# Optimization experiments

Measured on AMD Instinct MI355X. Metric: run time of the kernel, lower is better.

## Reference

```python
import jax, jax.numpy as jnp
import numpy as np

N_USERS = 100000
N_ITEMS = 50000
N_NODES = N_USERS + N_ITEMS
LATENT = 64
NNZ = 6000000
N_LAYERS = 3
BATCH = 2048


def setup_inputs() -> dict:
    key = jax.random.key(0)
    k1, k2, k3, k4, k5, k6, k7 = jax.random.split(key, 7)
    row_idx = jax.random.randint(k1, (NNZ,), 0, N_NODES, dtype=jnp.int64 if jax.config.jax_enable_x64 else jnp.int32)
    col_idx = jax.random.randint(k2, (NNZ,), 0, N_NODES, dtype=row_idx.dtype)
    vals = jax.random.uniform(k3, (NNZ,), dtype=jnp.float32) * (1.0 / 40.0)  # ~normalized adj weights
    user_emb = jax.random.normal(k4, (N_USERS, LATENT), dtype=jnp.float32) * 0.1
    item_emb = jax.random.normal(k5, (N_ITEMS, LATENT), dtype=jnp.float32) * 0.1
    users = jax.random.randint(k6, (BATCH,), 0, N_USERS, dtype=row_idx.dtype)
    items = jax.random.randint(k7, (BATCH,), 0, N_ITEMS, dtype=row_idx.dtype)
    return {"row_idx": row_idx, "col_idx": col_idx, "vals": vals,
            "user_emb": user_emb, "item_emb": item_emb,
            "users": users, "items": items}


def _spmm(row_idx, col_idx, vals, x):
    # sparse.mm(adj, x): out[r] += vals * x[c]
    contrib = vals[:, None] * x[col_idx]          # [nnz, d]
    return jax.ops.segment_sum(contrib, row_idx, num_segments=N_NODES)


def reference(row_idx, col_idx, vals, user_emb, item_emb, users, items):
    all_emb = jnp.concatenate([user_emb, item_emb], axis=0)   # [N, d]
    acc = all_emb
    emb = all_emb
    for _ in range(N_LAYERS):
        emb = _spmm(row_idx, col_idx, vals, emb)
        acc = acc + emb
    light_out = acc / (N_LAYERS + 1)                          # mean over layer outputs
    all_users = light_out[:N_USERS]
    all_items = light_out[N_USERS:]
    users_emb = all_users[users]                              # [B, d]
    items_emb = all_items[items]                              # [B, d]
    gamma = jnp.sum(users_emb * items_emb, axis=1)            # [B]
    return gamma
```

## Files before the change

kernel.cpp:

```cpp
#include <hip/hip_runtime.h>

#define N_USERS 100000
#define N_ITEMS 50000
#define N_NODES 150000
#define NNZ_C   6000000
#define LAT     64
#define BATCH   2048

#define BROWS2   256
#define NBUCK2   ((N_NODES + BROWS2 - 1) / BROWS2)
#define NBLK_A   256
#define CHUNK_A  ((NNZ_C + NBLK_A - 1) / NBLK_A)

__global__ __launch_bounds__(256) void k_zero(int* p, int n) {
    int i = blockIdx.x * blockDim.x + threadIdx.x;
    if (i < n) p[i] = 0;
}

__global__ __launch_bounds__(256) void k_bucket_count(const int* __restrict__ row,
                                                      int* __restrict__ bcnt) {
    __shared__ int h[NBUCK2];
    for (int k = threadIdx.x; k < NBUCK2; k += 256) h[k] = 0;
    __syncthreads();
    int beg = blockIdx.x * CHUNK_A;
    int end = min(beg + CHUNK_A, NNZ_C);
    for (int i = beg + threadIdx.x; i < end; i += 256)
        atomicAdd(&h[row[i] >> 8], 1);
    __syncthreads();
    for (int k = threadIdx.x; k < NBUCK2; k += 256) {
        int v = h[k];
        if (v) atomicAdd(&bcnt[k], v);
    }
}

__global__ __launch_bounds__(256) void k_bucket_scan(const int* __restrict__ bcnt,
                                                     int* __restrict__ bbase,
                                                     int* __restrict__ bcur,
                                                     int* __restrict__ row_ptr) {
    __shared__ int s[256];
    __shared__ int carry;
    int t = threadIdx.x;
    if (t == 0) carry = 0;
    __syncthreads();
    for (int c0 = 0; c0 < NBUCK2; c0 += 256) {
        int idx = c0 + t;
        int v = (idx < NBUCK2) ? bcnt[idx] : 0;
        s[t] = v; __syncthreads();
        for (int off = 1; off < 256; off <<= 1) {
            int x = (t >= off) ? s[t - off] : 0;
            __syncthreads();
            s[t] += x;
            __syncthreads();
        }
        int excl = carry + s[t] - v;
        if (idx < NBUCK2) { bbase[idx] = excl; bcur[idx] = excl; }
        __syncthreads();
        if (t == 255) carry += s[255];
        __syncthreads();
    }
    if (t == 0) { bbase[NBUCK2] = carry; row_ptr[N_NODES] = carry; }
}

__global__ __launch_bounds__(256) void k_bucket_scatter(const int* __restrict__ row,
                                                        const int* __restrict__ col,
                                                        const float* __restrict__ vals,
                                                        int* __restrict__ bcur,
                                                        int2* __restrict__ tmp) {
    __shared__ int h[NBUCK2];
    __shared__ int base[NBUCK2];
    for (int k = threadIdx.x; k < NBUCK2; k += 256) h[k] = 0;
    __syncthreads();
    int beg = blockIdx.x * CHUNK_A;
    int end = min(beg + CHUNK_A, NNZ_C);
    for (int i = beg + threadIdx.x; i < end; i += 256)
        atomicAdd(&h[row[i] >> 8], 1);
    __syncthreads();
    for (int k = threadIdx.x; k < NBUCK2; k += 256) {
        int v = h[k];
        base[k] = v ? atomicAdd(&bcur[k], v) : 0;
    }
    __syncthreads();
    for (int k = threadIdx.x; k < NBUCK2; k += 256) h[k] = 0;
    __syncthreads();
    for (int i = beg + threadIdx.x; i < end; i += 256) {
        int r = row[i];
        int b = r >> 8;
        int ofs = atomicAdd(&h[b], 1);
        int pos = base[b] + ofs;
        tmp[pos] = make_int2(((r & 255) << 18) | col[i],
                             __float_as_int(vals[i]));
    }
}

__global__ __launch_bounds__(256) void k_csr_build(const int* __restrict__ bbase,
                                                   const int2* __restrict__ tmp,
                                                   int2* __restrict__ edges,
                                                   int* __restrict__ row_ptr) {
    __shared__ int cnt[BROWS2];
    __shared__ int scn[BROWS2];
    __shared__ int cur[BROWS2];
    int b = blockIdx.x, t = threadIdx.x;
    int beg = bbase[b], end = bbase[b + 1];
    cnt[t] = 0;
    __syncthreads();
    for (int i = beg + t; i < end; i += 256)
        atomicAdd(&cnt[tmp[i].x >> 18], 1);
    __syncthreads();
    int v = cnt[t];
    scn[t] = v;
    __syncthreads();
    for (int off = 1; off < 256; off <<= 1) {
        int x = (t >= off) ? scn[t - off] : 0;
        __syncthreads();
        scn[t] += x;
        __syncthreads();
    }
    int excl = beg + scn[t] - v;
    cur[t] = excl;
    int g = b * BROWS2 + t;
    if (g < N_NODES) row_ptr[g] = excl;
    __syncthreads();
    for (int i = beg + t; i < end; i += 256) {
        int2 e = tmp[i];
        int pos = atomicAdd(&cur[e.x >> 18], 1);
        edges[pos] = make_int2(e.x & 0x3FFFF, e.y);
    }
}

template <bool SPLIT>
__global__ __launch_bounds__(256) void k_spmm(const int* __restrict__ row_ptr,
                                              const int2* __restrict__ edges,
                                              const float* __restrict__ x0,
                                              const float* __restrict__ x1,
                                              float* __restrict__ y) {
    int wv = (int)((blockIdx.x * blockDim.x + threadIdx.x) >> 6);
    int wave = __builtin_amdgcn_readfirstlane(wv);
    int lane = threadIdx.x & 63;
    if (wave >= N_NODES) return;
    int beg = row_ptr[wave], end = row_ptr[wave + 1];
    float a0 = 0.f, a1 = 0.f, a2 = 0.f, a3 = 0.f;
    auto xrow = [&](int c) -> const float* {
        if (SPLIT)
            return (c < N_USERS) ? x0 + ((size_t)c << 6)
                                 : x1 + ((size_t)(c - N_USERS) << 6);
        return x0 + ((size_t)c << 6);
    };
    int j = beg;
    for (; j + 4 <= end; j += 4) {
        int2 e0 = edges[j], e1 = edges[j + 1], e2 = edges[j + 2], e3 = edges[j + 3];
        a0 += __int_as_float(e0.y) * xrow(e0.x)[lane];
        a1 += __int_as_float(e1.y) * xrow(e1.x)[lane];
        a2 += __int_as_float(e2.y) * xrow(e2.x)[lane];
        a3 += __int_as_float(e3.y) * xrow(e3.x)[lane];
    }
    for (; j < end; ++j) {
        int2 e = edges[j];
        a0 += __int_as_float(e.y) * xrow(e.x)[lane];
    }
    y[((size_t)wave << 6) + lane] = (a0 + a1) + (a2 + a3);
}

__global__ __launch_bounds__(256) void k_spmm_sel(const int* __restrict__ row_ptr,
                                                  const int2* __restrict__ edges,
                                                  const float* __restrict__ x,
                                                  const int* __restrict__ users,
                                                  const int* __restrict__ items,
                                                  float* __restrict__ acc) {
    int w = (int)((blockIdx.x * blockDim.x + threadIdx.x) >> 6);
    int lane = threadIdx.x & 63;
    if (w >= 2 * BATCH) return;
    int node = (w < BATCH) ? users[w] : (N_USERS + items[w - BATCH]);
    node = __builtin_amdgcn_readfirstlane(node);
    int beg = row_ptr[node], end = row_ptr[node + 1];
    float a0 = 0.f, a1 = 0.f;
    int j = beg;
    for (; j + 2 <= end; j += 2) {
        int2 e0 = edges[j], e1 = edges[j + 1];
        a0 += __int_as_float(e0.y) * x[((size_t)e0.x << 6) + lane];
        a1 += __int_as_float(e1.y) * x[((size_t)e1.x << 6) + lane];
    }
    if (j < end) {
        int2 e = edges[j];
        a0 += __int_as_float(e.y) * x[((size_t)e.x << 6) + lane];
    }
    acc[w * LAT + lane] += a0 + a1;
}

__global__ __launch_bounds__(256) void k_accsel_init(const float* __restrict__ U,
                                                     const float* __restrict__ I,
                                                     const int* __restrict__ users,
                                                     const int* __restrict__ items,
                                                     float* __restrict__ acc) {
    int gid = blockIdx.x * blockDim.x + threadIdx.x;
    int w = gid >> 6, lane = threadIdx.x & 63;
    if (w >= 2 * BATCH) return;
    const float* src = (w < BATCH) ? U + ((size_t)users[w] << 6)
                                   : I + ((size_t)items[w - BATCH] << 6);
    acc[w * LAT + lane] = src[lane];
}

__global__ __launch_bounds__(256) void k_accsel_add(const float* __restrict__ emb,
                                                    const int* __restrict__ users,
                                                    const int* __restrict__ items,
                                                    float* acc) {
    int gid = blockIdx.x * blockDim.x + threadIdx.x;
    int w = gid >> 6, lane = threadIdx.x & 63;
    if (w >= 2 * BATCH) return;
    int node = (w < BATCH) ? users[w] : (N_USERS + items[w - BATCH]);
    acc[w * LAT + lane] += emb[(size_t)node * LAT + lane];
}

__global__ __launch_bounds__(256) void k_dot(const float* __restrict__ acc,
                                             float* __restrict__ out) {
    int gid = blockIdx.x * blockDim.x + threadIdx.x;
    int w = gid >> 6, lane = threadIdx.x & 63;
    if (w >= BATCH) return;
    float p = acc[w * LAT + lane] * acc[(BATCH + w) * LAT + lane];
    for (int off = 32; off > 0; off >>= 1) p += __shfl_down(p, off, 64);
    if (lane == 0) out[w] = p * (1.0f / 16.0f);
}

extern "C" void kernel_launch(void* const* d_in, const int* in_sizes, int n_in,
                              void* d_out, int out_size, void* d_ws, size_t ws_size,
                              hipStream_t stream) {
    const int*   row_idx  = (const int*)d_in[0];
    const int*   col_idx  = (const int*)d_in[1];
    const float* vals     = (const float*)d_in[2];
    const float* user_emb = (const float*)d_in[3];
    const float* item_emb = (const float*)d_in[4];
    const int*   users    = (const int*)d_in[5];
    const int*   items    = (const int*)d_in[6];
    float*       out      = (float*)d_out;

    char* ws = (char*)d_ws;
    size_t off = 0;
    auto alloc = [&](size_t bytes) -> void* {
        void* p = ws + off;
        off = (off + bytes + 255) & ~(size_t)255;
        return p;
    };
    int*   row_ptr = (int*)alloc((N_NODES + 1) * sizeof(int));
    int*   bcnt    = (int*)alloc(NBUCK2 * sizeof(int));
    int*   bbase   = (int*)alloc((NBUCK2 + 1) * sizeof(int));
    int*   bcur    = (int*)alloc(NBUCK2 * sizeof(int));
    int2*  edges   = (int2*)alloc((size_t)NNZ_C * sizeof(int2));
    float* embA    = (float*)alloc((size_t)N_NODES * LAT * sizeof(float));
    float* embB    = (float*)alloc((size_t)N_NODES * LAT * sizeof(float));
    float* acc     = (float*)alloc((size_t)2 * BATCH * LAT * sizeof(float));

    int2* tmp = (int2*)embA;

    k_zero<<<(NBUCK2 + 255) / 256, 256, 0, stream>>>(bcnt, NBUCK2);
    k_bucket_count<<<NBLK_A, 256, 0, stream>>>(row_idx, bcnt);
    k_bucket_scan<<<1, 256, 0, stream>>>(bcnt, bbase, bcur, row_ptr);
    k_bucket_scatter<<<NBLK_A, 256, 0, stream>>>(row_idx, col_idx, vals, bcur, tmp);
    k_csr_build<<<NBUCK2, 256, 0, stream>>>(bbase, tmp, edges, row_ptr);

    k_accsel_init<<<(2 * BATCH * 64) / 256, 256, 0, stream>>>(user_emb, item_emb,
                                                              users, items, acc);

    k_spmm<true><<<(N_NODES + 3) / 4, 256, 0, stream>>>(row_ptr, edges,
                                                        user_emb, item_emb, embA);
    k_accsel_add<<<(2 * BATCH * 64) / 256, 256, 0, stream>>>(embA, users, items, acc);

    k_spmm<false><<<(N_NODES + 3) / 4, 256, 0, stream>>>(row_ptr, edges,
                                                         embA, nullptr, embB);
    k_accsel_add<<<(2 * BATCH * 64) / 256, 256, 0, stream>>>(embB, users, items, acc);

    k_spmm_sel<<<(2 * BATCH * 64) / 256, 256, 0, stream>>>(row_ptr, edges, embB,
                                                           users, items, acc);

    k_dot<<<(BATCH * 64) / 256, 256, 0, stream>>>(acc, out);
}
```

Measured before the change: 796.0 us.

## Sub-sort CSR edges by column range within each row

The CSR build now bins each edge by its row plus the top bits of its column (32 column ranges per row), so edges inside a row are grouped by column region instead of landing in arbitrary atomic order. The intent is better cache locality for the gathered x rows during the SpMM layers. In exchange the build kernel uses 32x larger shared-memory histograms and adds a two-level scan, which raises build cost and may lower occupancy.

```diff
diff --git a/kernel.cpp b/kernel.cpp
--- a/kernel.cpp
+++ b/kernel.cpp
@@ -11,6 +11,8 @@
 #define NBUCK2   ((N_NODES + BROWS2 - 1) / BROWS2)
 #define NBLK_A   256
 #define CHUNK_A  ((NNZ_C + NBLK_A - 1) / NBLK_A)
+#define CBITS    5
+#define NBIN     (BROWS2 << CBITS)
 
 __global__ __launch_bounds__(256) void k_zero(int* p, int n) {
     int i = blockIdx.x * blockDim.x + threadIdx.x;
@@ -96,34 +98,50 @@
                                                    const int2* __restrict__ tmp,
                                                    int2* __restrict__ edges,
                                                    int* __restrict__ row_ptr) {
-    __shared__ int cnt[BROWS2];
-    __shared__ int scn[BROWS2];
-    __shared__ int cur[BROWS2];
+    __shared__ int cnt[NBIN];
+    __shared__ int scn[NBIN];
+    __shared__ int tsum[256];
     int b = blockIdx.x, t = threadIdx.x;
     int beg = bbase[b], end = bbase[b + 1];
-    cnt[t] = 0;
-    __syncthreads();
-    for (int i = beg + t; i < end; i += 256)
-        atomicAdd(&cnt[tmp[i].x >> 18], 1);
-    __syncthreads();
-    int v = cnt[t];
-    scn[t] = v;
+    #pragma unroll
+    for (int k = 0; k < NBIN / 256; ++k) cnt[t + k * 256] = 0;
+    __syncthreads();
+    for (int i = beg + t; i < end; i += 256) {
+        int key = tmp[i].x;
+        int bin = ((key >> 18) << CBITS) | ((key & 0x3FFFF) >> 13);
+        atomicAdd(&cnt[bin], 1);
+    }
+    __syncthreads();
+    int base_i = t * (NBIN / 256);
+    int s = 0;
+    #pragma unroll
+    for (int k = 0; k < NBIN / 256; ++k) s += cnt[base_i + k];
+    tsum[t] = s;
     __syncthreads();
     for (int off = 1; off < 256; off <<= 1) {
-        int x = (t >= off) ? scn[t - off] : 0;
-        __syncthreads();
-        scn[t] += x;
-        __syncthreads();
-    }
-    int excl = beg + scn[t] - v;
-    cur[t] = excl;
-    int g = b * BROWS2 + t;
-    if (g < N_NODES) row_ptr[g] = excl;
+        int x = (t >= off) ? tsum[t - off] : 0;
+        __syncthreads();
+        tsum[t] += x;
+        __syncthreads();
+    }
+    int run = tsum[t] - s;
+    #pragma unroll
+    for (int k = 0; k < NBIN / 256; ++k) {
+        scn[base_i + k] = run;
+        run += cnt[base_i + k];
+    }
+    __syncthreads();
+    {
+        int g = b * BROWS2 + t;
+        if (g < N_NODES) row_ptr[g] = beg + scn[t << CBITS];
+    }
     __syncthreads();
     for (int i = beg + t; i < end; i += 256) {
         int2 e = tmp[i];
-        int pos = atomicAdd(&cur[e.x >> 18], 1);
-        edges[pos] = make_int2(e.x & 0x3FFFF, e.y);
+        int col = e.x & 0x3FFFF;
+        int bin = ((e.x >> 18) << CBITS) | (col >> 13);
+        int pos = beg + atomicAdd(&scn[bin], 1);
+        edges[pos] = make_int2(col, e.y);
     }
 }
 
```

Result: slower. 842.9 us (+5.9%).
